# Kernel optimization log

Measured on AMD Instinct MI355X. Metric: run time of the kernel, lower is better.

## Reference

```python
import jax, jax.numpy as jnp
import numpy as np

SIM_THRESHOLD = 0.8


def setup_inputs() -> dict:
    key = jax.random.key(0)
    k1, k2, k3 = jax.random.split(key, 3)
    B, K = 256, 65536
    output = jax.random.normal(k1, (B, K + 1), dtype=jnp.float32)
    # cosine similarities in [-1, 1]
    cosine_similarities = jax.random.uniform(k2, (B, K), dtype=jnp.float32,
                                             minval=-1.0, maxval=1.0)
    target = jax.random.randint(k3, (B,), 0, 1)  # unused by the loss (label hardcoded to 0)
    return {"output": output, "cosine_similarities": cosine_similarities,
            "target": target}


def reference(output, cosine_similarities, target):
    # Per sample: keep logit 0 (positive) always; keep negative j iff cos_sim < threshold.
    # CE with label 0 on the masked logits == logsumexp(kept logits) - logit_0.
    # Masking with -inf reproduces masked_select exactly for the softmax/CE math,
    # without ragged shapes or a Python loop.
    B = output.shape[0]
    keep_neg = cosine_similarities < SIM_THRESHOLD            # [B, K]
    keep = jnp.concatenate([jnp.ones((B, 1), dtype=bool), keep_neg], axis=1)  # [B, K+1]
    masked_logits = jnp.where(keep, output, -jnp.inf)
    # loss_i = -log_softmax(masked_logits)[0] = logsumexp(masked) - logit_0
    losses = jax.nn.logsumexp(masked_logits, axis=1) - output[:, 0]
    return losses.mean()
```

## Files before the change

### kernel.cpp

```cpp
#include <hip/hip_runtime.h>

#define SIM_T 0.8f

__global__ __launch_bounds__(256) void pruner_partial(
    const float* __restrict__ out, const float* __restrict__ cs,
    float* __restrict__ ws, int K, int parts) {
  const int per_part = K / parts;
  const int row  = blockIdx.x / parts;
  const int part = blockIdx.x % parts;
  const int tid  = threadIdx.x;

  const float* crow = cs  + (size_t)row * K + (size_t)part * per_part;
  const float* orow = out + (size_t)row * (K + 1) + 1 + (size_t)part * per_part;

  float s0 = 0.f, s1 = 0.f, s2 = 0.f, s3 = 0.f;
  for (int k = tid * 4; k < per_part; k += 256 * 4) {
    float4 c = *reinterpret_cast<const float4*>(crow + k);
    float x0 = orow[k + 0];
    float x1 = orow[k + 1];
    float x2 = orow[k + 2];
    float x3 = orow[k + 3];
    s0 += (c.x < SIM_T) ? __expf(x0) : 0.0f;
    s1 += (c.y < SIM_T) ? __expf(x1) : 0.0f;
    s2 += (c.z < SIM_T) ? __expf(x2) : 0.0f;
    s3 += (c.w < SIM_T) ? __expf(x3) : 0.0f;
  }
  float s = (s0 + s1) + (s2 + s3);

  #pragma unroll
  for (int off = 32; off > 0; off >>= 1) s += __shfl_down(s, off, 64);

  __shared__ float lds[4];
  const int wave = tid >> 6;
  if ((tid & 63) == 0) lds[wave] = s;
  __syncthreads();
  if (tid == 0) ws[blockIdx.x] = (lds[0] + lds[1]) + (lds[2] + lds[3]);
}

__global__ __launch_bounds__(256) void pruner_final(
    const float* __restrict__ out, const float* __restrict__ ws,
    float* __restrict__ res, int K, int parts, int B) {
  const int i = threadIdx.x;
  float loss = 0.0f;
  if (i < B) {
    float t = 0.0f;
    for (int p = 0; p < parts; ++p) t += ws[i * parts + p];
    const float o0 = out[(size_t)i * (K + 1)];
    t += __expf(o0);
    loss = logf(t) - o0;
  }
  #pragma unroll
  for (int off = 32; off > 0; off >>= 1) loss += __shfl_down(loss, off, 64);

  __shared__ float lds[4];
  if ((i & 63) == 0) lds[i >> 6] = loss;
  __syncthreads();
  if (i == 0) res[0] = ((lds[0] + lds[1]) + (lds[2] + lds[3])) / (float)B;
}

extern "C" void kernel_launch(void* const* d_in, const int* in_sizes, int n_in,
                              void* d_out, int out_size, void* d_ws, size_t ws_size,
                              hipStream_t stream) {
  const float* out = (const float*)d_in[0];
  const float* cs  = (const float*)d_in[1];
  float* res = (float*)d_out;

  const int B = in_sizes[2];
  const int K = in_sizes[1] / B;
  const int PARTS = 8;

  float* ws = (float*)d_ws;

  pruner_partial<<<B * PARTS, 256, 0, stream>>>(out, cs, ws, K, PARTS);
  pruner_final<<<1, 256, 0, stream>>>(out, ws, res, K, PARTS, B);
}
```

Before: 28.22 us.

## Align output row loads to float4 via shifted masks staged in LDS

```diff
diff --git a/kernel.cpp b/kernel.cpp
--- a/kernel.cpp
+++ b/kernel.cpp
@@ -2,44 +2,102 @@
 
 #define SIM_T 0.8f
 
-__global__ __launch_bounds__(256) void pruner_partial(
+template <int NQ>
+__global__ __launch_bounds__(256) void pruner_partial_v4(
+    const float* __restrict__ out, const float* __restrict__ cs,
+    float* __restrict__ ws, int K, int parts, int B) {
+  const int per_part = NQ * 1024;
+  const int nquads   = per_part / 4;
+  const int row  = blockIdx.x / parts;
+  const int part = blockIdx.x % parts;
+  const int tid  = threadIdx.x;
+  const int d    = (-(row + 1)) & 3;
+
+  const float* crow  = cs  + (size_t)row * K + (size_t)part * per_part;
+  const float* obase = out + (size_t)row * (K + 1) + 1 + (size_t)part * per_part + d;
+
+  __shared__ unsigned int mask_w[(NQ * 256) / 4 + 1];
+
+  float4 ov[NQ];
+#pragma unroll
+  for (int i = 0; i < NQ; ++i) {
+    const int s = i * 256 + tid;
+    ov[i] = *reinterpret_cast<const float4*>(obase + 4 * s);
+  }
+  float4 cv[NQ];
+#pragma unroll
+  for (int i = 0; i < NQ; ++i) {
+    const int q = i * 256 + tid;
+    cv[i] = *reinterpret_cast<const float4*>(crow + 4 * q);
+  }
+  if (tid == 0) {
+    const float* pex = crow + per_part;
+    if (row == B - 1 && part == parts - 1) pex = crow + per_part - 4;
+    const float4 ce = *reinterpret_cast<const float4*>(pex);
+    const unsigned int nib = (ce.x < SIM_T ? 1u : 0u) | (ce.y < SIM_T ? 2u : 0u) |
+                             (ce.z < SIM_T ? 4u : 0u) | (ce.w < SIM_T ? 8u : 0u);
+    reinterpret_cast<unsigned char*>(mask_w)[nquads] = (unsigned char)nib;
+  }
+#pragma unroll
+  for (int i = 0; i < NQ; ++i) {
+    const int q = i * 256 + tid;
+    const unsigned int nib = (cv[i].x < SIM_T ? 1u : 0u) | (cv[i].y < SIM_T ? 2u : 0u) |
+                             (cv[i].z < SIM_T ? 4u : 0u) | (cv[i].w < SIM_T ? 8u : 0u);
+    reinterpret_cast<unsigned char*>(mask_w)[q] = (unsigned char)nib;
+  }
+  __syncthreads();
+
+  const bool lastpart = (part == parts - 1);
+  float a0 = 0.f, a1 = 0.f, a2 = 0.f, a3 = 0.f;
+#pragma unroll
+  for (int i = 0; i < NQ; ++i) {
+    const int s = i * 256 + tid;
+    const unsigned int w0 = mask_w[s >> 2];
+    const unsigned int w1 = mask_w[(s + 1) >> 2];
+    const unsigned int nib0 = (w0 >> ((s & 3) * 8)) & 0xFu;
+    const unsigned int nib1 = (w1 >> (((s + 1) & 3) * 8)) & 0xFu;
+    unsigned int m = ((nib0 >> d) | (nib1 << (4 - d))) & 0xFu;
+    if (lastpart && s == nquads - 1) m &= (0xFu >> d);
+    a0 += (m & 1u) ? __expf(ov[i].x) : 0.f;
+    a1 += (m & 2u) ? __expf(ov[i].y) : 0.f;
+    a2 += (m & 4u) ? __expf(ov[i].z) : 0.f;
+    a3 += (m & 8u) ? __expf(ov[i].w) : 0.f;
+  }
+  float s = (a0 + a1) + (a2 + a3);
+
+#pragma unroll
+  for (int off = 32; off > 0; off >>= 1) s += __shfl_down(s, off, 64);
+
+  __shared__ float lds[4];
+  if ((tid & 63) == 0) lds[tid >> 6] = s;
+  __syncthreads();
+  if (tid == 0) ws[blockIdx.x] = (lds[0] + lds[1]) + (lds[2] + lds[3]);
+}
+
+__global__ __launch_bounds__(256) void pruner_partial_simple(
     const float* __restrict__ out, const float* __restrict__ cs,
     float* __restrict__ ws, int K, int parts) {
   const int per_part = K / parts;
   const int row  = blockIdx.x / parts;
   const int part = blockIdx.x % parts;
   const int tid  = threadIdx.x;
-
   const float* crow = cs  + (size_t)row * K + (size_t)part * per_part;
   const float* orow = out + (size_t)row * (K + 1) + 1 + (size_t)part * per_part;
-
-  float s0 = 0.f, s1 = 0.f, s2 = 0.f, s3 = 0.f;
-  for (int k = tid * 4; k < per_part; k += 256 * 4) {
-    float4 c = *reinterpret_cast<const float4*>(crow + k);
-    float x0 = orow[k + 0];
-    float x1 = orow[k + 1];
-    float x2 = orow[k + 2];
-    float x3 = orow[k + 3];
-    s0 += (c.x < SIM_T) ? __expf(x0) : 0.0f;
-    s1 += (c.y < SIM_T) ? __expf(x1) : 0.0f;
-    s2 += (c.z < SIM_T) ? __expf(x2) : 0.0f;
-    s3 += (c.w < SIM_T) ? __expf(x3) : 0.0f;
-  }
-  float s = (s0 + s1) + (s2 + s3);
-
-  #pragma unroll
-  for (int off = 32; off > 0; off >>= 1) s += __shfl_down(s, off, 64);
-
+  float a = 0.f;
+  for (int k = tid; k < per_part; k += 256)
+    a += (crow[k] < SIM_T) ? __expf(orow[k]) : 0.f;
+#pragma unroll
+  for (int off = 32; off > 0; off >>= 1) a += __shfl_down(a, off, 64);
   __shared__ float lds[4];
-  const int wave = tid >> 6;
-  if ((tid & 63) == 0) lds[wave] = s;
+  if ((tid & 63) == 0) lds[tid >> 6] = a;
   __syncthreads();
   if (tid == 0) ws[blockIdx.x] = (lds[0] + lds[1]) + (lds[2] + lds[3]);
 }
 
 __global__ __launch_bounds__(256) void pruner_final(
-    const float* __restrict__ out, const float* __restrict__ ws,
-    float* __restrict__ res, int K, int parts, int B) {
+    const float* __restrict__ out, const float* __restrict__ cs,
+    const float* __restrict__ ws, float* __restrict__ res,
+    int K, int parts, int B, int head_in_final) {
   const int i = threadIdx.x;
   float loss = 0.0f;
   if (i < B) {
@@ -47,11 +105,18 @@
     for (int p = 0; p < parts; ++p) t += ws[i * parts + p];
     const float o0 = out[(size_t)i * (K + 1)];
     t += __expf(o0);
+    if (head_in_final) {
+      const int d = (-(i + 1)) & 3;
+      for (int j = 0; j < d; ++j) {
+        const float c = cs[(size_t)i * K + j];
+        const float x = out[(size_t)i * (K + 1) + 1 + j];
+        t += (c < SIM_T) ? __expf(x) : 0.f;
+      }
+    }
     loss = logf(t) - o0;
   }
-  #pragma unroll
+#pragma unroll
   for (int off = 32; off > 0; off >>= 1) loss += __shfl_down(loss, off, 64);
-
   __shared__ float lds[4];
   if ((i & 63) == 0) lds[i >> 6] = loss;
   __syncthreads();
@@ -67,10 +132,17 @@
 
   const int B = in_sizes[2];
   const int K = in_sizes[1] / B;
-  const int PARTS = 8;
-
   float* ws = (float*)d_ws;
 
-  pruner_partial<<<B * PARTS, 256, 0, stream>>>(out, cs, ws, K, PARTS);
-  pruner_final<<<1, 256, 0, stream>>>(out, ws, res, K, PARTS, B);
+  constexpr int NQ = 4;
+  const int chunk = NQ * 1024;
+  if (B <= 256 && K % chunk == 0) {
+    const int parts = K / chunk;
+    pruner_partial_v4<NQ><<<B * parts, 256, 0, stream>>>(out, cs, ws, K, parts, B);
+    pruner_final<<<1, 256, 0, stream>>>(out, cs, ws, res, K, parts, B, 1);
+  } else {
+    const int parts = 8;
+    pruner_partial_simple<<<B * parts, 256, 0, stream>>>(out, cs, ws, K, parts);
+    pruner_final<<<1, 256, 0, stream>>>(out, cs, ws, res, K, parts, B, 0);
+  }
 }
```

Result: slower. 30.51 us (+8.1%).
